# Kernel tuning notes

Hardware: AMD Instinct MI355X
Metric: run time of the kernel (lower is better)

## Reference

```python
import jax, jax.numpy as jnp
import numpy as np

EPS = 1e-6  # fast_transformers CausalLinearAttention eps
HEADS = 8
HEAD_DIM = 16  # embed_dim 128 / heads 8


def _causal_linear(Q, K, V):
    """Causal linear attention numerator via KV cumulative outer-product scan.
    Q, K: (B, L, H, E); V: (B, L, H, Ev). Returns (B, L, H, Ev)."""
    Qs = jnp.swapaxes(Q, 0, 1)  # (L, B, H, E)
    Ks = jnp.swapaxes(K, 0, 1)
    Vs = jnp.swapaxes(V, 0, 1)
    B, H, E = Q.shape[0], Q.shape[2], Q.shape[3]
    Ev = V.shape[3]
    S0 = jnp.zeros((B, H, E, Ev), dtype=Q.dtype)

    def step(S, qkv):
        q, k, v = qkv  # each (B, H, E)
        S = S + k[..., :, None] * v[..., None, :]  # accumulate outer(k, v)
        o = jnp.einsum('bhe,bhef->bhf', q, S)
        return S, o

    _, out = jax.lax.scan(step, S0, (Qs, Ks, Vs))  # out: (L, B, H, Ev)
    return jnp.swapaxes(out, 0, 1)


def setup_inputs() -> dict:
    key = jax.random.key(0)
    ks = jax.random.split(key, 4)
    F = 128
    query = jax.random.normal(ks[0], (8, 512, 64, F), dtype=jnp.float32)
    scale = 1.0 / np.sqrt(F)
    Wq = jax.random.normal(ks[1], (F, HEADS * HEAD_DIM), dtype=jnp.float32) * scale
    Wk = jax.random.normal(ks[2], (F, HEADS * HEAD_DIM), dtype=jnp.float32) * scale
    Wv = jax.random.normal(ks[3], (F, HEADS * HEAD_DIM), dtype=jnp.float32) * scale
    bq = jnp.zeros((HEADS * HEAD_DIM,), jnp.float32)  # bias_initializer='zeros'
    bk = jnp.zeros((HEADS * HEAD_DIM,), jnp.float32)
    bv = jnp.zeros((HEADS * HEAD_DIM,), jnp.float32)
    return {"query": query, "Wq": Wq, "bq": bq, "Wk": Wk, "bk": bk, "Wv": Wv, "bv": bv}


def reference(query, Wq, bq, Wk, bk, Wv, bv):
    # query: (B, L, N, F); dim=1 is the attended (time) axis.
    B, L, N, F = query.shape
    H, E = HEADS, HEAD_DIM
    x = jnp.swapaxes(query, 1, 2)  # (B, N, L, F); key = value = query
    q = (x @ Wq + bq).reshape(B * N, L, H, E)
    k = (x @ Wk + bk).reshape(B * N, L, H, E)
    v = (x @ Wv + bv).reshape(B * N, L, H, E)
    # feature map phi(x) = elu(x) + 1
    Qf = jax.nn.elu(q) + 1.0
    Kf = jax.nn.elu(k) + 1.0  # LengthMask([1],1) is all-ones -> no-op
    # normalizer: Z_i = 1 / (phi(q_i) . sum_{j<=i} phi(k_j) + eps)
    Z = 1.0 / (jnp.einsum('blhe,blhe->blh', Qf, jnp.cumsum(Kf, axis=1)) + EPS)
    out = _causal_linear(Qf, Kf, v) * Z[..., None]  # (B*N, L, H, E)
    out = out.reshape(B, N, L, H * E)
    return jnp.swapaxes(out, 1, 2)  # (B, L, N, out_channels)
```

## Files before the change

### kernel.cpp

```cpp
#include <hip/hip_runtime.h>
#include <hip/hip_bf16.h>
#include <math.h>

#define BDIM 8
#define LDIM 512
#define NDIM 64
#define FDIM 128
#define HDIM 8
#define EDIM 16
#define CH 64
#define NCHUNK (LDIM / CH)
#define EPSV 1e-6f

typedef __attribute__((ext_vector_type(8))) short bf16x8;
typedef __attribute__((ext_vector_type(4))) float f32x4;

__device__ __forceinline__ float phi_elu1(float x) {
    return x > 0.f ? x + 1.f : __expf(x);
}
__device__ __forceinline__ float bf2f(short s) {
    union { unsigned u; float f; } un;
    un.u = ((unsigned)(unsigned short)s) << 16;
    return un.f;
}

__global__ __launch_bounds__(256, 3)
void cla_chunked_kernel(const float* __restrict__ query,
                        const float* __restrict__ Wq, const float* __restrict__ bq,
                        const float* __restrict__ Wk, const float* __restrict__ bk,
                        const float* __restrict__ Wv, const float* __restrict__ bv,
                        float* __restrict__ out)
{
    __shared__ __align__(16) __hip_bfloat16 Wt[48][136];
    __shared__ __align__(16) unsigned char xsSc[CH * 136 * 2];
    __shared__ __align__(16) __hip_bfloat16 Qf[CH][40];
    __shared__ __align__(16) __hip_bfloat16 Kf[CH][40];
    __shared__ __align__(16) __hip_bfloat16 KfT[16][72];
    __shared__ __align__(16) __hip_bfloat16 VfT[16][72];
    __shared__ float Sst[16][17];
    __shared__ float KsumL[16];
    __shared__ float rsL[CH];
    __shared__ float bsL[48];

    const int tid = threadIdx.x;
    const int s = blockIdx.x >> 3;
    const int h = blockIdx.x & 7;
    const int b = s >> 6;
    const int n = s & 63;

    __hip_bfloat16* xs = (__hip_bfloat16*)xsSc;
    __hip_bfloat16* Sc = (__hip_bfloat16*)xsSc;

    for (int idx = tid; idx < 48 * FDIM; idx += 256) {
        int e16 = idx & 15;
        int kk  = (idx >> 4) & 127;
        int m   = idx >> 11;
        const float* Wm = (m == 0) ? Wq : (m == 1) ? Wk : Wv;
        Wt[m * 16 + e16][kk] = __float2bfloat16(Wm[kk * FDIM + h * EDIM + e16]);
    }
    if (tid < 48) {
        const float* bm = (tid < 16) ? bq : (tid < 32) ? bk : bv;
        bsL[tid] = bm[h * EDIM + (tid & 15)];
    }
    for (int idx = tid; idx < CH * 16; idx += 256) {
        int rr = idx >> 4, cc = idx & 15;
        Qf[rr][16 + cc] = __float2bfloat16(0.f);
        Kf[rr][16 + cc] = __float2bfloat16(0.f);
    }
    for (int idx = tid; idx < 16 * 17; idx += 256) ((float*)Sst)[idx] = 0.f;
    if (tid < 16) KsumL[tid] = 0.f;

    const int lid  = tid & 63;
    const int w    = tid >> 6;
    const int mrow = lid & 15;
    const int koff = (lid >> 4) * 8;
    const int r0   = (lid >> 4) * 4;

    __syncthreads();

    for (int c = 0; c < NCHUNK; ++c) {
        const int l0 = c * CH;

        for (int v = tid; v < CH * 32; v += 256) {
            int row = v >> 5;
            int c4  = v & 31;
            const float4 xv = *(const float4*)(query
                + (((size_t)b * LDIM + l0 + row) * NDIM + n) * FDIM + c4 * 4);
            __hip_bfloat16* xr = xs + row * 136 + c4 * 4;
            xr[0] = __float2bfloat16(xv.x);
            xr[1] = __float2bfloat16(xv.y);
            xr[2] = __float2bfloat16(xv.z);
            xr[3] = __float2bfloat16(xv.w);
        }
        __syncthreads();

        #pragma unroll
        for (int nt = 0; nt < 3; ++nt) {
            f32x4 acc = {0.f, 0.f, 0.f, 0.f};
            #pragma unroll
            for (int kq = 0; kq < 4; ++kq) {
                bf16x8 a  = *(const bf16x8*)(xs + (16 * w + mrow) * 136 + kq * 32 + koff);
                bf16x8 bb = *(const bf16x8*)&Wt[nt * 16 + mrow][kq * 32 + koff];
                acc = __builtin_amdgcn_mfma_f32_16x16x32_bf16(a, bb, acc, 0, 0, 0);
            }
            const float bias = bsL[nt * 16 + mrow];
            #pragma unroll
            for (int r = 0; r < 4; ++r) {
                const int row = 16 * w + r0 + r;
                float val = acc[r] + bias;
                if (nt == 0) {
                    Qf[row][mrow] = __float2bfloat16(phi_elu1(val));
                } else if (nt == 1) {
                    __hip_bfloat16 kb = __float2bfloat16(phi_elu1(val));
                    Kf[row][mrow] = kb;
                    KfT[mrow][row] = kb;
                } else {
                    VfT[mrow][row] = __float2bfloat16(val);
                }
            }
        }
        __syncthreads();

        {
            float rsacc[4] = {0.f, 0.f, 0.f, 0.f};
            for (int nt = 0; nt <= w; ++nt) {
                f32x4 sacc = {0.f, 0.f, 0.f, 0.f};
                bf16x8 a  = *(const bf16x8*)&Qf[16 * w + mrow][koff];
                bf16x8 bb = *(const bf16x8*)&Kf[16 * nt + mrow][koff];
                sacc = __builtin_amdgcn_mfma_f32_16x16x32_bf16(a, bb, sacc, 0, 0, 0);
                #pragma unroll
                for (int r = 0; r < 4; ++r) {
                    const int gi = 16 * w + r0 + r;
                    const int gj = 16 * nt + mrow;
                    float val = (gj <= gi) ? sacc[r] : 0.f;
                    Sc[gi * 72 + gj] = __float2bfloat16(val);
                    rsacc[r] += val;
                }
            }
            if (w == 0 || w == 2) {
                const int rr = 16 * w + (lid >> 2);
                const int cc = 16 * (w + 1) + (lid & 3) * 4;
                *(uint2*)&Sc[rr * 72 + cc] = (uint2){0u, 0u};
            }
            #pragma unroll
            for (int r = 0; r < 4; ++r) {
                float p = rsacc[r];
                p += __shfl_xor(p, 1);
                p += __shfl_xor(p, 2);
                p += __shfl_xor(p, 4);
                p += __shfl_xor(p, 8);
                if (mrow == 0) rsL[16 * w + r0 + r] = p;
            }
        }
        __syncthreads();

        f32x4 oacc = {0.f, 0.f, 0.f, 0.f};
        const int nmf = (w <= 1) ? 1 : 2;
        for (int kc = 0; kc < nmf; ++kc) {
            bf16x8 a  = *(const bf16x8*)&Sc[(16 * w + mrow) * 72 + kc * 32 + koff];
            bf16x8 bb = *(const bf16x8*)&VfT[mrow][kc * 32 + koff];
            oacc = __builtin_amdgcn_mfma_f32_16x16x32_bf16(a, bb, oacc, 0, 0, 0);
        }
        f32x4 dsacc = {0.f, 0.f, 0.f, 0.f};
        if (w == 0) {
            #pragma unroll
            for (int kc = 0; kc < 2; ++kc) {
                bf16x8 a  = *(const bf16x8*)&KfT[mrow][kc * 32 + koff];
                bf16x8 bb = *(const bf16x8*)&VfT[mrow][kc * 32 + koff];
                dsacc = __builtin_amdgcn_mfma_f32_16x16x32_bf16(a, bb, dsacc, 0, 0, 0);
            }
        }
        {
            float Sv[16], Kv[16];
            #pragma unroll
            for (int e = 0; e < 16; ++e) {
                Sv[e] = Sst[e][mrow];
                Kv[e] = KsumL[e];
            }
            #pragma unroll
            for (int r = 0; r < 4; ++r) {
                const int gi = 16 * w + r0 + r;
                bf16x8 qa = *(const bf16x8*)&Qf[gi][0];
                bf16x8 qb = *(const bf16x8*)&Qf[gi][8];
                float oi = 0.f, di = 0.f;
                #pragma unroll
                for (int j = 0; j < 8; ++j) {
                    float qv = bf2f(qa[j]);
                    oi = fmaf(qv, Sv[j], oi);
                    di = fmaf(qv, Kv[j], di);
                }
                #pragma unroll
                for (int j = 0; j < 8; ++j) {
                    float qv = bf2f(qb[j]);
                    oi = fmaf(qv, Sv[8 + j], oi);
                    di = fmaf(qv, Kv[8 + j], di);
                }
                const float o = oacc[r] + oi;
                const float d = rsL[gi] + di + EPSV;
                out[(((size_t)b * LDIM + l0 + gi) * NDIM + n) * (HDIM * EDIM) + h * EDIM + mrow] = o / d;
            }
        }
        __syncthreads();

        if (w == 0) {
            #pragma unroll
            for (int r = 0; r < 4; ++r) Sst[r0 + r][mrow] += dsacc[r];
        }
        if (w == 1 && lid < 16) {
            float ssum = 0.f;
            const bf16x8* kp = (const bf16x8*)&KfT[lid][0];
            #pragma unroll
            for (int j = 0; j < 8; ++j) {
                bf16x8 kv8 = kp[j];
                #pragma unroll
                for (int t = 0; t < 8; ++t) ssum += bf2f(kv8[t]);
            }
            KsumL[lid] += ssum;
        }
        __syncthreads();
    }
}

extern "C" void kernel_launch(void* const* d_in, const int* in_sizes, int n_in,
                              void* d_out, int out_size, void* d_ws, size_t ws_size,
                              hipStream_t stream) {
    const float* query = (const float*)d_in[0];
    const float* Wq = (const float*)d_in[1];
    const float* bq = (const float*)d_in[2];
    const float* Wk = (const float*)d_in[3];
    const float* bk = (const float*)d_in[4];
    const float* Wv = (const float*)d_in[5];
    const float* bv = (const float*)d_in[6];
    float* out = (float*)d_out;

    dim3 grid(512 * 8);
    dim3 block(256);
    hipLaunchKernelGGL(cla_chunked_kernel, grid, block, 0, stream,
                       query, Wq, bq, Wk, bk, Wv, bv, out);
}
```

Baseline: 539.0 us.

## Split chunked linear attention into projection, state-scan, and per-chunk attention kernels

Replaces the single fused kernel, which walked sequence chunks serially per (sequence, head) block, with three kernels. The first projects Q/K/V once per chunk for all heads into bf16 workspace buffers, reading the input once instead of once per head. The second computes per-chunk prefix KV states and key sums. The third handles each (sequence, head, chunk) independently, giving many more parallel blocks. This trades extra global-memory round trips and launches for less redundant input reading and a shorter serial dependency chain. The old fused kernel is kept as a fallback when the workspace is too small.

```diff
diff --git a/kernel.cpp b/kernel.cpp
--- a/kernel.cpp
+++ b/kernel.cpp
@@ -22,6 +22,215 @@
     union { unsigned u; float f; } un;
     un.u = ((unsigned)(unsigned short)s) << 16;
     return un.f;
+}
+__device__ __forceinline__ short f2bf(float x) {
+    __hip_bfloat16 h = __float2bfloat16(x);
+    union { __hip_bfloat16 h; short s; } un;
+    un.h = h;
+    return un.s;
+}
+
+__global__ __launch_bounds__(256, 3)
+void cla_proj(const float* __restrict__ query,
+              const float* __restrict__ Wq, const float* __restrict__ bq,
+              const float* __restrict__ Wk, const float* __restrict__ bk,
+              const float* __restrict__ Wv, const float* __restrict__ bv,
+              short* __restrict__ wsQ, short* __restrict__ wsK, short* __restrict__ wsV)
+{
+    __shared__ __align__(16) __hip_bfloat16 xs[CH][136];
+    const int tid = threadIdx.x;
+    const int s = blockIdx.x >> 3;
+    const int c = blockIdx.x & 7;
+    const int b = s >> 6, n = s & 63;
+    const int l0 = c * CH;
+    const int lid = tid & 63, w = tid >> 6;
+    const int mrow = lid & 15, koff = (lid >> 4) * 8, r0 = (lid >> 4) * 4;
+
+    for (int v = tid; v < CH * 32; v += 256) {
+        int row = v >> 5, c4 = v & 31;
+        float4 xv = *(const float4*)(query + (((size_t)b * LDIM + l0 + row) * NDIM + n) * FDIM + c4 * 4);
+        __hip_bfloat16* xr = &xs[row][c4 * 4];
+        xr[0] = __float2bfloat16(xv.x); xr[1] = __float2bfloat16(xv.y);
+        xr[2] = __float2bfloat16(xv.z); xr[3] = __float2bfloat16(xv.w);
+    }
+    __syncthreads();
+
+    bf16x8 Af[4][4];
+    #pragma unroll
+    for (int rt = 0; rt < 4; ++rt)
+        #pragma unroll
+        for (int kq = 0; kq < 4; ++kq)
+            Af[rt][kq] = *(const bf16x8*)&xs[16 * rt + mrow][kq * 32 + koff];
+
+    #pragma unroll 1
+    for (int ct = 0; ct < 6; ++ct) {
+        const int tci = 6 * w + ct;
+        const int m = tci >> 3, hh = tci & 7;
+        const float* Wm = (m == 0) ? Wq : (m == 1) ? Wk : Wv;
+        const float* bm = (m == 0) ? bq : (m == 1) ? bk : bv;
+        bf16x8 Wf[4];
+        #pragma unroll
+        for (int kq = 0; kq < 4; ++kq)
+            #pragma unroll
+            for (int j = 0; j < 8; ++j)
+                Wf[kq][j] = f2bf(Wm[(kq * 32 + koff + j) * FDIM + hh * 16 + mrow]);
+        f32x4 acc[4];
+        #pragma unroll
+        for (int rt = 0; rt < 4; ++rt) acc[rt] = (f32x4){0.f, 0.f, 0.f, 0.f};
+        #pragma unroll
+        for (int kq = 0; kq < 4; ++kq)
+            #pragma unroll
+            for (int rt = 0; rt < 4; ++rt)
+                acc[rt] = __builtin_amdgcn_mfma_f32_16x16x32_bf16(Af[rt][kq], Wf[kq], acc[rt], 0, 0, 0);
+        const float bias = bm[hh * 16 + mrow];
+        short* dst = ((m == 0) ? wsQ : (m == 1) ? wsK : wsV)
+                     + ((size_t)(s * 8 + hh) * LDIM + l0) * 16;
+        #pragma unroll
+        for (int rt = 0; rt < 4; ++rt)
+            #pragma unroll
+            for (int r = 0; r < 4; ++r) {
+                int gi = 16 * rt + r0 + r;
+                float val = acc[rt][r] + bias;
+                if (m < 2) val = phi_elu1(val);
+                dst[gi * 16 + mrow] = f2bf(val);
+            }
+    }
+}
+
+__global__ __launch_bounds__(64, 4)
+void cla_state(const short* __restrict__ wsK, const short* __restrict__ wsV,
+               float* __restrict__ Spre, float* __restrict__ Kpre)
+{
+    const int tid = threadIdx.x;
+    const int sh = blockIdx.x;
+    const int mrow = tid & 15, koff = (tid >> 4) * 8, r0 = (tid >> 4) * 4;
+    const short* pk = wsK + (size_t)sh * LDIM * 16;
+    const short* pv = wsV + (size_t)sh * LDIM * 16;
+    float Srun[4] = {0.f, 0.f, 0.f, 0.f};
+    float Krun = 0.f;
+    for (int c = 0; c < NCHUNK; ++c) {
+        float* sp = Spre + ((size_t)sh * NCHUNK + c) * 256;
+        #pragma unroll
+        for (int r = 0; r < 4; ++r) sp[(r0 + r) * 16 + mrow] = Srun[r];
+        if (tid < 16) Kpre[((size_t)sh * NCHUNK + c) * 16 + tid] = Krun;
+        f32x4 ds = {0.f, 0.f, 0.f, 0.f};
+        float kp = 0.f;
+        #pragma unroll
+        for (int kc = 0; kc < 2; ++kc) {
+            bf16x8 ka, vb;
+            #pragma unroll
+            for (int j = 0; j < 8; ++j) {
+                int idx = (c * CH + kc * 32 + koff + j) * 16 + mrow;
+                ka[j] = pk[idx];
+                vb[j] = pv[idx];
+            }
+            ds = __builtin_amdgcn_mfma_f32_16x16x32_bf16(ka, vb, ds, 0, 0, 0);
+            #pragma unroll
+            for (int j = 0; j < 8; ++j) kp += bf2f(ka[j]);
+        }
+        kp += __shfl_xor(kp, 16);
+        kp += __shfl_xor(kp, 32);
+        Krun += kp;
+        #pragma unroll
+        for (int r = 0; r < 4; ++r) Srun[r] += ds[r];
+    }
+}
+
+__global__ __launch_bounds__(256, 4)
+void cla_attn(const short* __restrict__ wsQ, const short* __restrict__ wsK,
+              const short* __restrict__ wsV, const float* __restrict__ SpreG,
+              const float* __restrict__ KpreG, float* __restrict__ out)
+{
+    __shared__ __align__(16) __hip_bfloat16 Qf[CH][40];
+    __shared__ __align__(16) __hip_bfloat16 Kf[CH][40];
+    __shared__ __align__(16) __hip_bfloat16 VfT[16][72];
+    __shared__ __align__(16) __hip_bfloat16 Sc[CH][72];
+    __shared__ float Sp[16][17];
+    __shared__ float ks[16];
+
+    const int tid = threadIdx.x;
+    const int bi = blockIdx.x;
+    const int s = bi >> 6, h = (bi >> 3) & 7, c = bi & 7;
+    const int b = s >> 6, n = s & 63;
+    const int l0 = c * CH;
+    const size_t base = ((size_t)(s * 8 + h) * LDIM + l0) * 16;
+
+    if (tid < 128) {
+        int row = tid >> 1, half = tid & 1;
+        *(uint4*)&Qf[row][half * 8] = *(const uint4*)(wsQ + base + row * 16 + half * 8);
+        *(uint4*)&Qf[row][16 + half * 8] = (uint4){0u, 0u, 0u, 0u};
+    } else {
+        int t = tid - 128, row = t >> 1, half = t & 1;
+        *(uint4*)&Kf[row][half * 8] = *(const uint4*)(wsK + base + row * 16 + half * 8);
+        *(uint4*)&Kf[row][16 + half * 8] = (uint4){0u, 0u, 0u, 0u};
+    }
+    {
+        int row = tid >> 2, part = tid & 3;
+        uint2 vv = *(const uint2*)(wsV + base + row * 16 + part * 4);
+        const short* vs = (const short*)&vv;
+        #pragma unroll
+        for (int jj = 0; jj < 4; ++jj)
+            *(short*)&VfT[part * 4 + jj][row] = vs[jj];
+    }
+    Sp[tid >> 4][tid & 15] = SpreG[((size_t)(s * 8 + h) * NCHUNK + c) * 256 + tid];
+    if (tid < 16) ks[tid] = KpreG[((size_t)(s * 8 + h) * NCHUNK + c) * 16 + tid];
+    __syncthreads();
+
+    const int lid = tid & 63, w = tid >> 6;
+    const int mrow = lid & 15, koff = (lid >> 4) * 8, r0 = (lid >> 4) * 4;
+
+    float rs[4];
+    {
+        float rsacc[4] = {0.f, 0.f, 0.f, 0.f};
+        bf16x8 qa = *(const bf16x8*)&Qf[16 * w + mrow][koff];
+        for (int nt = 0; nt <= w; ++nt) {
+            f32x4 sacc = {0.f, 0.f, 0.f, 0.f};
+            bf16x8 kb = *(const bf16x8*)&Kf[16 * nt + mrow][koff];
+            sacc = __builtin_amdgcn_mfma_f32_16x16x32_bf16(qa, kb, sacc, 0, 0, 0);
+            #pragma unroll
+            for (int r = 0; r < 4; ++r) {
+                int gi = 16 * w + r0 + r, gj = 16 * nt + mrow;
+                float val = (gj <= gi) ? sacc[r] : 0.f;
+                *(short*)&Sc[gi][gj] = f2bf(val);
+                rsacc[r] += val;
+            }
+        }
+        if (w == 0 || w == 2) {
+            int rr = 16 * w + (lid >> 2), cc = 16 * (w + 1) + (lid & 3) * 4;
+            *(uint2*)&Sc[rr][cc] = (uint2){0u, 0u};
+        }
+        #pragma unroll
+        for (int r = 0; r < 4; ++r) {
+            float p = rsacc[r];
+            p += __shfl_xor(p, 1); p += __shfl_xor(p, 2);
+            p += __shfl_xor(p, 4); p += __shfl_xor(p, 8);
+            rs[r] = p;
+        }
+    }
+
+    f32x4 oacc = {0.f, 0.f, 0.f, 0.f};
+    const int nmf = (w <= 1) ? 1 : 2;
+    for (int kc = 0; kc < nmf; ++kc) {
+        bf16x8 a  = *(const bf16x8*)&Sc[16 * w + mrow][kc * 32 + koff];
+        bf16x8 bb = *(const bf16x8*)&VfT[mrow][kc * 32 + koff];
+        oacc = __builtin_amdgcn_mfma_f32_16x16x32_bf16(a, bb, oacc, 0, 0, 0);
+    }
+    float Sv[16], Kv[16];
+    #pragma unroll
+    for (int e = 0; e < 16; ++e) { Sv[e] = Sp[e][mrow]; Kv[e] = ks[e]; }
+    #pragma unroll
+    for (int r = 0; r < 4; ++r) {
+        int gi = 16 * w + r0 + r;
+        bf16x8 qa = *(const bf16x8*)&Qf[gi][0];
+        bf16x8 qb = *(const bf16x8*)&Qf[gi][8];
+        float oi = 0.f, di = 0.f;
+        #pragma unroll
+        for (int j = 0; j < 8; ++j) { float qv = bf2f(qa[j]); oi = fmaf(qv, Sv[j], oi); di = fmaf(qv, Kv[j], di); }
+        #pragma unroll
+        for (int j = 0; j < 8; ++j) { float qv = bf2f(qb[j]); oi = fmaf(qv, Sv[8 + j], oi); di = fmaf(qv, Kv[8 + j], di); }
+        float o = oacc[r] + oi, d = rs[r] + di + EPSV;
+        out[(((size_t)b * LDIM + l0 + gi) * NDIM + n) * (HDIM * EDIM) + h * 16 + mrow] = o / d;
+    }
 }
 
 __global__ __launch_bounds__(256, 3)
@@ -80,7 +289,6 @@
 
     for (int c = 0; c < NCHUNK; ++c) {
         const int l0 = c * CH;
-
         for (int v = tid; v < CH * 32; v += 256) {
             int row = v >> 5;
             int c4  = v & 31;
@@ -233,8 +441,25 @@
     const float* bv = (const float*)d_in[6];
     float* out = (float*)d_out;
 
-    dim3 grid(512 * 8);
-    dim3 block(256);
-    hipLaunchKernelGGL(cla_chunked_kernel, grid, block, 0, stream,
-                       query, Wq, bq, Wk, bk, Wv, bv, out);
-}
+    const size_t QKV = (size_t)512 * 8 * 512 * 16;
+    const size_t SPRE = (size_t)512 * 8 * 8 * 256;
+    const size_t KPRE = (size_t)512 * 8 * 8 * 16;
+    const size_t need = QKV * 3 * 2 + SPRE * 4 + KPRE * 4;
+
+    if (ws_size >= need) {
+        short* wsQ = (short*)d_ws;
+        short* wsK = wsQ + QKV;
+        short* wsV = wsK + QKV;
+        float* Spre = (float*)(wsV + QKV);
+        float* Kpre = Spre + SPRE;
+        hipLaunchKernelGGL(cla_proj, dim3(4096), dim3(256), 0, stream,
+                           query, Wq, bq, Wk, bk, Wv, bv, wsQ, wsK, wsV);
+        hipLaunchKernelGGL(cla_state, dim3(4096), dim3(64), 0, stream,
+                           wsK, wsV, Spre, Kpre);
+        hipLaunchKernelGGL(cla_attn, dim3(32768), dim3(256), 0, stream,
+                           wsQ, wsK, wsV, Spre, Kpre, out);
+    } else {
+        hipLaunchKernelGGL(cla_chunked_kernel, dim3(4096), dim3(256), 0, stream,
+                           query, Wq, bq, Wk, bk, Wv, bv, out);
+    }
+}
```

Measured after the change: 445.3 us. 17.4% less time.
